# Kernel tuning notes

Measured on AMD Instinct MI355X. Metric: run time of the kernel, lower is better.

The kernel has to match this reference:

```python
import jax, jax.numpy as jnp
import numpy as np

N = 4096
D_IN = 1024
D_OUT = 1024
NUM_HEADS = 16
HEAD_DIM = D_OUT // NUM_HEADS


def setup_inputs() -> dict:
    key = jax.random.key(0)
    ks = jax.random.split(key, 7)
    scale = 1.0 / np.sqrt(D_IN)
    return {
        "q": jax.random.normal(ks[0], (N, D_IN), dtype=jnp.float32),
        "k": jax.random.normal(ks[1], (N, D_IN), dtype=jnp.float32),
        "v": jax.random.normal(ks[2], (N, D_IN), dtype=jnp.float32),
        "W_q": jax.random.normal(ks[3], (D_IN, D_OUT), dtype=jnp.float32) * scale,
        "W_k": jax.random.normal(ks[4], (D_IN, D_OUT), dtype=jnp.float32) * scale,
        "W_v": jax.random.normal(ks[5], (D_IN, D_OUT), dtype=jnp.float32) * scale,
        "W_o": jax.random.normal(ks[6], (D_OUT, D_OUT), dtype=jnp.float32) * scale,
    }


def reference(q, k, v, W_q, W_k, W_v, W_o):
    n = q.shape[0]
    # QKV projections -> [h, n, d]
    Q = (q @ W_q).reshape(n, NUM_HEADS, HEAD_DIM).transpose(1, 0, 2)
    K = (k @ W_k).reshape(n, NUM_HEADS, HEAD_DIM).transpose(1, 0, 2)
    V = (v @ W_v).reshape(n, NUM_HEADS, HEAD_DIM).transpose(1, 0, 2)
    scores = jnp.einsum('hid,hjd->hij', Q, K) / jnp.sqrt(jnp.float32(HEAD_DIM))
    attn = jax.nn.softmax(scores, axis=-1)  # dropout p=0.0 (eval) -> no-op
    h = jnp.einsum('hij,hjd->hid', attn, V)
    h = h.transpose(1, 0, 2).reshape(n, D_OUT)
    return h @ W_o
```

## Files before the change

### kernel.cpp

```cpp
#include <hip/hip_runtime.h>
#include <math.h>

#define NTOK   4096
#define DMODEL 1024
#define NHEADS 16
#define HDIM   64
#define KDIM   1024

typedef __attribute__((ext_vector_type(8))) short          bf16x8;
typedef __attribute__((ext_vector_type(4))) float          f32x4;
typedef __attribute__((ext_vector_type(4))) unsigned short us4;

static __device__ __forceinline__ unsigned short f2bf(float f) {
    unsigned int u = __float_as_uint(f);
    u += 0x7fffu + ((u >> 16) & 1u);
    return (unsigned short)(u >> 16);
}

static __device__ __forceinline__ unsigned int pkbf(float a, float b) {
    unsigned int ua = __float_as_uint(a) + 0x8000u;
    unsigned int ub = __float_as_uint(b) + 0x8000u;
    return __builtin_amdgcn_perm(ub, ua, 0x07060302u);
}

#if __has_builtin(__builtin_amdgcn_exp2f)
#define EXP2(x) __builtin_amdgcn_exp2f(x)
#else
#define EXP2(x) exp2f(x)
#endif

static __device__ __forceinline__ void async_copy16(void* lds, const void* g) {
    __builtin_amdgcn_global_load_lds(
        (const __attribute__((address_space(1))) unsigned int*)g,
        (__attribute__((address_space(3))) unsigned int*)lds, 16, 0, 0);
}

__global__ __launch_bounds__(256)
void cast_wt_kernel(const float* __restrict__ Wq, const float* __restrict__ Wk,
                    const float* __restrict__ Wv, const float* __restrict__ Wo,
                    unsigned short* __restrict__ Tq, unsigned short* __restrict__ Tk,
                    unsigned short* __restrict__ Tv, unsigned short* __restrict__ To) {
    __shared__ float Ws[64][65];
    const float* W;
    unsigned short* T;
    switch (blockIdx.z) {
        case 0:  W = Wq; T = Tq; break;
        case 1:  W = Wk; T = Tk; break;
        case 2:  W = Wv; T = Tv; break;
        default: W = Wo; T = To; break;
    }
    const int k0 = blockIdx.x * 64, n0 = blockIdx.y * 64;
    const int t = threadIdx.x;
    #pragma unroll
    for (int i = 0; i < 4; i++) {
        int c  = i * 256 + t;
        int kk = c >> 4;
        int n4 = (c & 15) << 2;
        *(float4*)(&Ws[kk][n4]) =
            *(const float4*)(W + (size_t)(k0 + kk) * DMODEL + n0 + n4);
    }
    __syncthreads();
    #pragma unroll
    for (int i = 0; i < 4; i++) {
        int c  = i * 256 + t;
        int nn = c >> 4;
        int k4 = (c & 15) << 2;
        us4 o = { f2bf(Ws[k4 + 0][nn]), f2bf(Ws[k4 + 1][nn]),
                  f2bf(Ws[k4 + 2][nn]), f2bf(Ws[k4 + 3][nn]) };
        *(us4*)(T + (size_t)(n0 + nn) * KDIM + k0 + k4) = o;
    }
}

__global__ __launch_bounds__(256, 3)
void qkv_gemm(const float* __restrict__ Aq, const float* __restrict__ Ak,
              const float* __restrict__ Av,
              const unsigned short* __restrict__ Btq,
              const unsigned short* __restrict__ Btk,
              const unsigned short* __restrict__ Btv,
              unsigned short* __restrict__ Oq, unsigned short* __restrict__ Ok,
              unsigned short* __restrict__ Ov) {
    __shared__ unsigned short As[128 * 64];
    __shared__ unsigned short Bs[128 * 64];

    const float* A;
    const unsigned short* Bt;
    unsigned short* Out;
    int mode;
    float sc;
    switch (blockIdx.z) {
        case 0:  A = Aq; Bt = Btq; Out = Oq; mode = 1; sc = 0.18033688011112042f; break;
        case 1:  A = Ak; Bt = Btk; Out = Ok; mode = 1; sc = 1.0f;   break;
        default: A = Av; Bt = Btv; Out = Ov; mode = 2; sc = 1.0f;   break;
    }

    const int t    = threadIdx.x;
    const int w    = t >> 6;
    const int lane = t & 63;
    const int quad = lane >> 4;
    const int l15  = lane & 15;
    const int wr   = w >> 1, wc = w & 1;
    const int bm   = blockIdx.y * 128, bn = blockIdx.x * 128;

    f32x4 acc[4][4];
    #pragma unroll
    for (int i = 0; i < 4; i++)
        #pragma unroll
        for (int j = 0; j < 4; j++) acc[i][j] = (f32x4)(0.f);

    for (int k0 = 0; k0 < KDIM; k0 += 64) {
        __syncthreads();
        #pragma unroll
        for (int i = 0; i < 4; i++) {
            int cb = (i * 4 + w) * 64;
            int c  = cb + lane;
            int r  = c >> 3;
            int ko = (c & 7) * 8;
            async_copy16((void*)(Bs + cb * 8),
                         (const void*)(Bt + (size_t)(bn + r) * KDIM + k0 + ko));
        }
        #pragma unroll
        for (int i = 0; i < 4; i++) {
            int c2 = i * 256 + t;
            int r  = c2 >> 3;
            int k8 = (c2 & 7) * 8;
            const float* src = A + (size_t)(bm + r) * KDIM + k0 + k8;
            float4 f0 = *(const float4*)(src);
            float4 f1 = *(const float4*)(src + 4);
            bf16x8 pk = { (short)f2bf(f0.x), (short)f2bf(f0.y),
                          (short)f2bf(f0.z), (short)f2bf(f0.w),
                          (short)f2bf(f1.x), (short)f2bf(f1.y),
                          (short)f2bf(f1.z), (short)f2bf(f1.w) };
            *(bf16x8*)(As + r * 64 + k8) = pk;
        }
        __syncthreads();
        #pragma unroll
        for (int kq = 0; kq < 2; kq++) {
            bf16x8 af[4], bf[4];
            #pragma unroll
            for (int mt = 0; mt < 4; mt++)
                af[mt] = *(bf16x8*)(As + (wr * 64 + mt * 16 + l15) * 64 + kq * 32 + quad * 8);
            #pragma unroll
            for (int nt = 0; nt < 4; nt++)
                bf[nt] = *(bf16x8*)(Bs + (wc * 64 + nt * 16 + l15) * 64 + kq * 32 + quad * 8);
            #pragma unroll
            for (int mt = 0; mt < 4; mt++)
                #pragma unroll
                for (int nt = 0; nt < 4; nt++)
                    acc[mt][nt] = __builtin_amdgcn_mfma_f32_16x16x32_bf16(
                        af[mt], bf[nt], acc[mt][nt], 0, 0, 0);
        }
    }

    #pragma unroll
    for (int mt = 0; mt < 4; mt++) {
        #pragma unroll
        for (int nt = 0; nt < 4; nt++) {
            int col  = bn + wc * 64 + nt * 16 + l15;
            int row0 = bm + wr * 64 + mt * 16 + quad * 4;
            if (mode == 1) {
                size_t base = ((size_t)(col >> 6)) * NTOK * HDIM + (col & 63);
                #pragma unroll
                for (int r = 0; r < 4; r++)
                    Out[base + (size_t)(row0 + r) * HDIM] = f2bf(acc[mt][nt][r] * sc);
            } else {
                size_t base = ((size_t)(col >> 6)) * HDIM * NTOK +
                              (size_t)(col & 63) * NTOK + row0;
                us4 o = { f2bf(acc[mt][nt][0]), f2bf(acc[mt][nt][1]),
                          f2bf(acc[mt][nt][2]), f2bf(acc[mt][nt][3]) };
                *(us4*)(Out + base) = o;
            }
        }
    }
}

__global__ __launch_bounds__(256, 3)
void out_gemm(const unsigned short* __restrict__ A,
              const unsigned short* __restrict__ Bt,
              float* __restrict__ Out) {
    __shared__ unsigned short As[128 * 64];
    __shared__ unsigned short Bs[128 * 64];

    const int t    = threadIdx.x;
    const int w    = t >> 6;
    const int lane = t & 63;
    const int quad = lane >> 4;
    const int l15  = lane & 15;
    const int wr   = w >> 1, wc = w & 1;
    const int bm   = blockIdx.y * 128, bn = blockIdx.x * 128;

    f32x4 acc[4][4];
    #pragma unroll
    for (int i = 0; i < 4; i++)
        #pragma unroll
        for (int j = 0; j < 4; j++) acc[i][j] = (f32x4)(0.f);

    for (int k0 = 0; k0 < KDIM; k0 += 64) {
        __syncthreads();
        #pragma unroll
        for (int i = 0; i < 4; i++) {
            int cb = (i * 4 + w) * 64;
            int c  = cb + lane;
            int r  = c >> 3;
            int ko = (c & 7) * 8;
            async_copy16((void*)(Bs + cb * 8),
                         (const void*)(Bt + (size_t)(bn + r) * KDIM + k0 + ko));
            async_copy16((void*)(As + cb * 8),
                         (const void*)(A + (size_t)(bm + r) * KDIM + k0 + ko));
        }
        __syncthreads();
        #pragma unroll
        for (int kq = 0; kq < 2; kq++) {
            bf16x8 af[4], bf[4];
            #pragma unroll
            for (int mt = 0; mt < 4; mt++)
                af[mt] = *(bf16x8*)(As + (wr * 64 + mt * 16 + l15) * 64 + kq * 32 + quad * 8);
            #pragma unroll
            for (int nt = 0; nt < 4; nt++)
                bf[nt] = *(bf16x8*)(Bs + (wc * 64 + nt * 16 + l15) * 64 + kq * 32 + quad * 8);
            #pragma unroll
            for (int mt = 0; mt < 4; mt++)
                #pragma unroll
                for (int nt = 0; nt < 4; nt++)
                    acc[mt][nt] = __builtin_amdgcn_mfma_f32_16x16x32_bf16(
                        af[mt], bf[nt], acc[mt][nt], 0, 0, 0);
        }
    }

    #pragma unroll
    for (int mt = 0; mt < 4; mt++) {
        #pragma unroll
        for (int nt = 0; nt < 4; nt++) {
            int col  = bn + wc * 64 + nt * 16 + l15;
            int row0 = bm + wr * 64 + mt * 16 + quad * 4;
            #pragma unroll
            for (int r = 0; r < 4; r++)
                Out[(size_t)(row0 + r) * DMODEL + col] = acc[mt][nt][r];
        }
    }
}

__global__ __launch_bounds__(256)
void attn_mfma(const unsigned short* __restrict__ Q,
               const unsigned short* __restrict__ K,
               const unsigned short* __restrict__ Vt,
               unsigned short* __restrict__ ctx) {
    __shared__ __align__(16) unsigned short Ks[2 * 4096];
    __shared__ __align__(16) unsigned short Vs[2 * 4096];
    __shared__ __align__(16) unsigned short Ps[4][32][72];

    const int h    = blockIdx.y;
    const int qt   = blockIdx.x;
    const int t    = threadIdx.x;
    const int w    = t >> 6;
    const int lane = t & 63;
    const int quad = lane >> 4;
    const int l15  = lane & 15;

    const unsigned short* Qg =
        Q + ((size_t)h * NTOK + qt * 128 + w * 32 + l15) * HDIM;
    bf16x8 qf[2][2];
    qf[0][0] = *(const bf16x8*)(Qg + quad * 8);
    qf[0][1] = *(const bf16x8*)(Qg + 32 + quad * 8);
    qf[1][0] = *(const bf16x8*)(Qg + 16 * HDIM + quad * 8);
    qf[1][1] = *(const bf16x8*)(Qg + 16 * HDIM + 32 + quad * 8);

    const unsigned short* Kg = K  + (size_t)h * NTOK * HDIM;
    const unsigned short* Vg = Vt + (size_t)h * HDIM * NTOK;

    const int xb = l15 & 7;
    const int a0 = l15 * 64 + ((quad    ) ^ xb) * 8;
    const int a1 = l15 * 64 + ((quad + 4) ^ xb) * 8;

    auto stage = [&](int kt, int b) {
        #pragma unroll
        for (int i = 0; i < 2; i++) {
            int c = i * 256 + t;
            int r = c >> 3;
            int o = ((c & 7) ^ (r & 7)) * 8;
            async_copy16((void*)(Ks + b * 4096 + (i * 256 + w * 64) * 8),
                         (const void*)(Kg + (size_t)(kt * 64 + r) * HDIM + o));
            async_copy16((void*)(Vs + b * 4096 + (i * 256 + w * 64) * 8),
                         (const void*)(Vg + (size_t)r * NTOK + kt * 64 + o));
        }
    };

    f32x4 O[2][4];
    float l_part[2] = {0.f, 0.f};
    #pragma unroll
    for (int tl = 0; tl < 2; tl++)
        #pragma unroll
        for (int dt = 0; dt < 4; dt++) O[tl][dt] = (f32x4)(0.f);

    stage(0, 0);

    for (int kt = 0; kt < NTOK / 64; kt++) {
        const int cur = kt & 1;
        __syncthreads();
        if (kt + 1 < NTOK / 64) stage(kt + 1, cur ^ 1);

        f32x4 s[2][4];
        #pragma unroll
        for (int kc = 0; kc < 4; kc++) {
            bf16x8 kf0 = *(bf16x8*)(Ks + cur * 4096 + kc * 1024 + a0);
            bf16x8 kf1 = *(bf16x8*)(Ks + cur * 4096 + kc * 1024 + a1);
            #pragma unroll
            for (int tl = 0; tl < 2; tl++) {
                f32x4 acc = (f32x4)(0.f);
                acc = __builtin_amdgcn_mfma_f32_16x16x32_bf16(kf0, qf[tl][0], acc, 0, 0, 0);
                acc = __builtin_amdgcn_mfma_f32_16x16x32_bf16(kf1, qf[tl][1], acc, 0, 0, 0);
                s[tl][kc] = acc;
            }
        }

        #pragma unroll
        for (int tl = 0; tl < 2; tl++) {
            float sm = 0.f;
            #pragma unroll
            for (int kc = 0; kc < 4; kc++) {
                float e0 = EXP2(s[tl][kc][0]);
                float e1 = EXP2(s[tl][kc][1]);
                float e2 = EXP2(s[tl][kc][2]);
                float e3 = EXP2(s[tl][kc][3]);
                sm += (e0 + e1) + (e2 + e3);
                uint2 p = { pkbf(e0, e1), pkbf(e2, e3) };
                *(uint2*)(&Ps[w][tl * 16 + l15][kc * 16 + quad * 4]) = p;
            }
            l_part[tl] += sm;
        }
        asm volatile("s_waitcnt lgkmcnt(0)" ::: "memory");

        bf16x8 pf[2][2];
        #pragma unroll
        for (int tl = 0; tl < 2; tl++) {
            pf[tl][0] = *(bf16x8*)(&Ps[w][tl * 16 + l15][quad * 8]);
            pf[tl][1] = *(bf16x8*)(&Ps[w][tl * 16 + l15][32 + quad * 8]);
        }
        #pragma unroll
        for (int dt = 0; dt < 4; dt++) {
            bf16x8 vf0 = *(bf16x8*)(Vs + cur * 4096 + dt * 1024 + a0);
            bf16x8 vf1 = *(bf16x8*)(Vs + cur * 4096 + dt * 1024 + a1);
            #pragma unroll
            for (int tl = 0; tl < 2; tl++) {
                O[tl][dt] = __builtin_amdgcn_mfma_f32_16x16x32_bf16(vf0, pf[tl][0], O[tl][dt], 0, 0, 0);
                O[tl][dt] = __builtin_amdgcn_mfma_f32_16x16x32_bf16(vf1, pf[tl][1], O[tl][dt], 0, 0, 0);
            }
        }
    }

    #pragma unroll
    for (int tl = 0; tl < 2; tl++) {
        float ls = l_part[tl];
        ls += __shfl_xor(ls, 16, 64);
        ls += __shfl_xor(ls, 32, 64);
        float inv = 1.f / ls;
        size_t row = (size_t)qt * 128 + w * 32 + tl * 16 + l15;
        #pragma unroll
        for (int dt = 0; dt < 4; dt++) {
            uint2 o = { pkbf(O[tl][dt][0] * inv, O[tl][dt][1] * inv),
                        pkbf(O[tl][dt][2] * inv, O[tl][dt][3] * inv) };
            *(uint2*)(ctx + row * DMODEL + h * HDIM + dt * 16 + quad * 4) = o;
        }
    }
}

extern "C" void kernel_launch(void* const* d_in, const int* in_sizes, int n_in,
                              void* d_out, int out_size, void* d_ws, size_t ws_size,
                              hipStream_t stream) {
    const float* q  = (const float*)d_in[0];
    const float* k  = (const float*)d_in[1];
    const float* v  = (const float*)d_in[2];
    const float* Wq = (const float*)d_in[3];
    const float* Wk = (const float*)d_in[4];
    const float* Wv = (const float*)d_in[5];
    const float* Wo = (const float*)d_in[6];
    float* out = (float*)d_out;

    unsigned short* WqT = (unsigned short*)d_ws;
    unsigned short* WkT = WqT + (size_t)DMODEL * KDIM;
    unsigned short* WvT = WkT + (size_t)DMODEL * KDIM;
    unsigned short* WoT = WvT + (size_t)DMODEL * KDIM;
    unsigned short* Qh  = WoT + (size_t)DMODEL * KDIM;
    unsigned short* Kh  = Qh  + (size_t)NTOK * DMODEL;
    unsigned short* Vth = Kh  + (size_t)NTOK * DMODEL;
    unsigned short* ctx = Vth + (size_t)NTOK * DMODEL;

    cast_wt_kernel<<<dim3(16, 16, 4), 256, 0, stream>>>(Wq, Wk, Wv, Wo,
                                                        WqT, WkT, WvT, WoT);
    qkv_gemm<<<dim3(DMODEL / 128, NTOK / 128, 3), 256, 0, stream>>>(
        q, k, v, WqT, WkT, WvT, Qh, Kh, Vth);
    attn_mfma<<<dim3(NTOK / 128, NHEADS), 256, 0, stream>>>(Qh, Kh, Vth, ctx);
    out_gemm<<<dim3(DMODEL / 128, NTOK / 128), 256, 0, stream>>>(ctx, WoT, out);
}
```

Before: 296.1 us.

## Precast activations to bf16, use hardware bf16 pack, MFMA row sums in attention

Adds a separate cast kernel that converts q/k/v to bf16 so the QKV GEMM can load its A tiles with async global-to-LDS copies instead of converting in registers. This path is only taken when the workspace is large enough. Packed bf16 conversion now uses the hardware cvt_pk builtin where the compiler provides it. In attention, the softmax row sums are computed with an MFMA against a ones vector instead of scalar adds and shuffles, the K/V staging addresses are simplified, and V fragments are preloaded with per-tile waits. The cost is an extra kernel launch plus a round trip of the activations through bf16 memory.

```diff
diff --git a/kernel.cpp b/kernel.cpp
--- a/kernel.cpp
+++ b/kernel.cpp
@@ -17,10 +17,15 @@
     return (unsigned short)(u >> 16);
 }
 
-static __device__ __forceinline__ unsigned int pkbf(float a, float b) {
+static __device__ __forceinline__ unsigned int pk2bf(float a, float b) {
+#if __has_builtin(__builtin_amdgcn_cvt_pk_bf16_f32)
+    return __builtin_bit_cast(unsigned int,
+                              __builtin_amdgcn_cvt_pk_bf16_f32(a, b));
+#else
     unsigned int ua = __float_as_uint(a) + 0x8000u;
     unsigned int ub = __float_as_uint(b) + 0x8000u;
     return __builtin_amdgcn_perm(ub, ua, 0x07060302u);
+#endif
 }
 
 #if __has_builtin(__builtin_amdgcn_exp2f)
@@ -71,26 +76,49 @@
     }
 }
 
+__global__ __launch_bounds__(256)
+void cast_in_kernel(const float* __restrict__ q, const float* __restrict__ k,
+                    const float* __restrict__ v,
+                    unsigned short* __restrict__ Qb,
+                    unsigned short* __restrict__ Kb,
+                    unsigned short* __restrict__ Vb) {
+    const float* src;
+    unsigned short* dst;
+    switch (blockIdx.y) {
+        case 0:  src = q; dst = Qb; break;
+        case 1:  src = k; dst = Kb; break;
+        default: src = v; dst = Vb; break;
+    }
+    size_t i = ((size_t)blockIdx.x * 256 + threadIdx.x) * 8;
+    float4 f0 = *(const float4*)(src + i);
+    float4 f1 = *(const float4*)(src + i + 4);
+    uint2 o0 = { pk2bf(f0.x, f0.y), pk2bf(f0.z, f0.w) };
+    uint2 o1 = { pk2bf(f1.x, f1.y), pk2bf(f1.z, f1.w) };
+    *(uint2*)(dst + i)     = o0;
+    *(uint2*)(dst + i + 4) = o1;
+}
+
 __global__ __launch_bounds__(256, 3)
-void qkv_gemm(const float* __restrict__ Aq, const float* __restrict__ Ak,
-              const float* __restrict__ Av,
-              const unsigned short* __restrict__ Btq,
-              const unsigned short* __restrict__ Btk,
-              const unsigned short* __restrict__ Btv,
-              unsigned short* __restrict__ Oq, unsigned short* __restrict__ Ok,
-              unsigned short* __restrict__ Ov) {
+void qkv_gemm_pre(const unsigned short* __restrict__ Qb,
+                  const unsigned short* __restrict__ Kb,
+                  const unsigned short* __restrict__ Vb,
+                  const unsigned short* __restrict__ Btq,
+                  const unsigned short* __restrict__ Btk,
+                  const unsigned short* __restrict__ Btv,
+                  unsigned short* __restrict__ Oq, unsigned short* __restrict__ Ok,
+                  unsigned short* __restrict__ Ov) {
     __shared__ unsigned short As[128 * 64];
     __shared__ unsigned short Bs[128 * 64];
 
-    const float* A;
+    const unsigned short* A;
     const unsigned short* Bt;
     unsigned short* Out;
     int mode;
     float sc;
     switch (blockIdx.z) {
-        case 0:  A = Aq; Bt = Btq; Out = Oq; mode = 1; sc = 0.18033688011112042f; break;
-        case 1:  A = Ak; Bt = Btk; Out = Ok; mode = 1; sc = 1.0f;   break;
-        default: A = Av; Bt = Btv; Out = Ov; mode = 2; sc = 1.0f;   break;
+        case 0:  A = Qb; Bt = Btq; Out = Oq; mode = 1; sc = 0.18033688011112042f; break;
+        case 1:  A = Kb; Bt = Btk; Out = Ok; mode = 1; sc = 1.0f; break;
+        default: A = Vb; Bt = Btv; Out = Ov; mode = 2; sc = 1.0f; break;
     }
 
     const int t    = threadIdx.x;
@@ -117,20 +145,8 @@
             int ko = (c & 7) * 8;
             async_copy16((void*)(Bs + cb * 8),
                          (const void*)(Bt + (size_t)(bn + r) * KDIM + k0 + ko));
-        }
-        #pragma unroll
-        for (int i = 0; i < 4; i++) {
-            int c2 = i * 256 + t;
-            int r  = c2 >> 3;
-            int k8 = (c2 & 7) * 8;
-            const float* src = A + (size_t)(bm + r) * KDIM + k0 + k8;
-            float4 f0 = *(const float4*)(src);
-            float4 f1 = *(const float4*)(src + 4);
-            bf16x8 pk = { (short)f2bf(f0.x), (short)f2bf(f0.y),
-                          (short)f2bf(f0.z), (short)f2bf(f0.w),
-                          (short)f2bf(f1.x), (short)f2bf(f1.y),
-                          (short)f2bf(f1.z), (short)f2bf(f1.w) };
-            *(bf16x8*)(As + r * 64 + k8) = pk;
+            async_copy16((void*)(As + cb * 8),
+                         (const void*)(A + (size_t)(bm + r) * KDIM + k0 + ko));
         }
         __syncthreads();
         #pragma unroll
@@ -174,6 +190,107 @@
 }
 
 __global__ __launch_bounds__(256, 3)
+void qkv_gemm(const float* __restrict__ Aq, const float* __restrict__ Ak,
+              const float* __restrict__ Av,
+              const unsigned short* __restrict__ Btq,
+              const unsigned short* __restrict__ Btk,
+              const unsigned short* __restrict__ Btv,
+              unsigned short* __restrict__ Oq, unsigned short* __restrict__ Ok,
+              unsigned short* __restrict__ Ov) {
+    __shared__ unsigned short As[128 * 64];
+    __shared__ unsigned short Bs[128 * 64];
+
+    const float* A;
+    const unsigned short* Bt;
+    unsigned short* Out;
+    int mode;
+    float sc;
+    switch (blockIdx.z) {
+        case 0:  A = Aq; Bt = Btq; Out = Oq; mode = 1; sc = 0.18033688011112042f; break;
+        case 1:  A = Ak; Bt = Btk; Out = Ok; mode = 1; sc = 1.0f; break;
+        default: A = Av; Bt = Btv; Out = Ov; mode = 2; sc = 1.0f; break;
+    }
+
+    const int t    = threadIdx.x;
+    const int w    = t >> 6;
+    const int lane = t & 63;
+    const int quad = lane >> 4;
+    const int l15  = lane & 15;
+    const int wr   = w >> 1, wc = w & 1;
+    const int bm   = blockIdx.y * 128, bn = blockIdx.x * 128;
+
+    f32x4 acc[4][4];
+    #pragma unroll
+    for (int i = 0; i < 4; i++)
+        #pragma unroll
+        for (int j = 0; j < 4; j++) acc[i][j] = (f32x4)(0.f);
+
+    for (int k0 = 0; k0 < KDIM; k0 += 64) {
+        __syncthreads();
+        #pragma unroll
+        for (int i = 0; i < 4; i++) {
+            int cb = (i * 4 + w) * 64;
+            int c  = cb + lane;
+            int r  = c >> 3;
+            int ko = (c & 7) * 8;
+            async_copy16((void*)(Bs + cb * 8),
+                         (const void*)(Bt + (size_t)(bn + r) * KDIM + k0 + ko));
+        }
+        #pragma unroll
+        for (int i = 0; i < 4; i++) {
+            int c2 = i * 256 + t;
+            int r  = c2 >> 3;
+            int k8 = (c2 & 7) * 8;
+            const float* src = A + (size_t)(bm + r) * KDIM + k0 + k8;
+            float4 f0 = *(const float4*)(src);
+            float4 f1 = *(const float4*)(src + 4);
+            uint2 p0 = { pk2bf(f0.x, f0.y), pk2bf(f0.z, f0.w) };
+            uint2 p1 = { pk2bf(f1.x, f1.y), pk2bf(f1.z, f1.w) };
+            *(uint2*)(As + r * 64 + k8)     = p0;
+            *(uint2*)(As + r * 64 + k8 + 4) = p1;
+        }
+        __syncthreads();
+        #pragma unroll
+        for (int kq = 0; kq < 2; kq++) {
+            bf16x8 af[4], bf[4];
+            #pragma unroll
+            for (int mt = 0; mt < 4; mt++)
+                af[mt] = *(bf16x8*)(As + (wr * 64 + mt * 16 + l15) * 64 + kq * 32 + quad * 8);
+            #pragma unroll
+            for (int nt = 0; nt < 4; nt++)
+                bf[nt] = *(bf16x8*)(Bs + (wc * 64 + nt * 16 + l15) * 64 + kq * 32 + quad * 8);
+            #pragma unroll
+            for (int mt = 0; mt < 4; mt++)
+                #pragma unroll
+                for (int nt = 0; nt < 4; nt++)
+                    acc[mt][nt] = __builtin_amdgcn_mfma_f32_16x16x32_bf16(
+                        af[mt], bf[nt], acc[mt][nt], 0, 0, 0);
+        }
+    }
+
+    #pragma unroll
+    for (int mt = 0; mt < 4; mt++) {
+        #pragma unroll
+        for (int nt = 0; nt < 4; nt++) {
+            int col  = bn + wc * 64 + nt * 16 + l15;
+            int row0 = bm + wr * 64 + mt * 16 + quad * 4;
+            if (mode == 1) {
+                size_t base = ((size_t)(col >> 6)) * NTOK * HDIM + (col & 63);
+                #pragma unroll
+                for (int r = 0; r < 4; r++)
+                    Out[base + (size_t)(row0 + r) * HDIM] = f2bf(acc[mt][nt][r] * sc);
+            } else {
+                size_t base = ((size_t)(col >> 6)) * HDIM * NTOK +
+                              (size_t)(col & 63) * NTOK + row0;
+                us4 o = { f2bf(acc[mt][nt][0]), f2bf(acc[mt][nt][1]),
+                          f2bf(acc[mt][nt][2]), f2bf(acc[mt][nt][3]) };
+                *(us4*)(Out + base) = o;
+            }
+        }
+    }
+}
+
+__global__ __launch_bounds__(256, 3)
 void out_gemm(const unsigned short* __restrict__ A,
               const unsigned short* __restrict__ Bt,
               float* __restrict__ Out) {
@@ -267,29 +384,37 @@
     const unsigned short* Kg = K  + (size_t)h * NTOK * HDIM;
     const unsigned short* Vg = Vt + (size_t)h * HDIM * NTOK;
 
+    const int rr = t >> 3;
+    const int oo = ((t & 7) ^ (rr & 7)) * 8;
+    const unsigned short* kbase = Kg + (size_t)rr * HDIM + oo;
+    const unsigned short* vbase = Vg + (size_t)rr * NTOK + oo;
+    unsigned short* ksd = Ks + w * 512;
+    unsigned short* vsd = Vs + w * 512;
+
+    auto stage = [&](int kt, int b) {
+        const unsigned short* kp = kbase + (size_t)kt * 64 * HDIM;
+        const unsigned short* vp = vbase + kt * 64;
+        async_copy16((void*)(ksd + b * 4096),        (const void*)kp);
+        async_copy16((void*)(ksd + b * 4096 + 2048), (const void*)(kp + 32 * HDIM));
+        async_copy16((void*)(vsd + b * 4096),        (const void*)vp);
+        async_copy16((void*)(vsd + b * 4096 + 2048), (const void*)(vp + (size_t)32 * NTOK));
+    };
+
     const int xb = l15 & 7;
     const int a0 = l15 * 64 + ((quad    ) ^ xb) * 8;
     const int a1 = l15 * 64 + ((quad + 4) ^ xb) * 8;
 
-    auto stage = [&](int kt, int b) {
-        #pragma unroll
-        for (int i = 0; i < 2; i++) {
-            int c = i * 256 + t;
-            int r = c >> 3;
-            int o = ((c & 7) ^ (r & 7)) * 8;
-            async_copy16((void*)(Ks + b * 4096 + (i * 256 + w * 64) * 8),
-                         (const void*)(Kg + (size_t)(kt * 64 + r) * HDIM + o));
-            async_copy16((void*)(Vs + b * 4096 + (i * 256 + w * 64) * 8),
-                         (const void*)(Vg + (size_t)r * NTOK + kt * 64 + o));
-        }
-    };
+    const bf16x8 ones = { 16256, 16256, 16256, 16256,
+                          16256, 16256, 16256, 16256 };
 
     f32x4 O[2][4];
-    float l_part[2] = {0.f, 0.f};
-    #pragma unroll
-    for (int tl = 0; tl < 2; tl++)
+    f32x4 lacc[2];
+    #pragma unroll
+    for (int tl = 0; tl < 2; tl++) {
+        lacc[tl] = (f32x4)(0.f);
         #pragma unroll
         for (int dt = 0; dt < 4; dt++) O[tl][dt] = (f32x4)(0.f);
+    }
 
     stage(0, 0);
 
@@ -312,52 +437,46 @@
             }
         }
 
+        bf16x8 vf[4][2];
+        #pragma unroll
+        for (int dt = 0; dt < 4; dt++) {
+            vf[dt][0] = *(bf16x8*)(Vs + cur * 4096 + dt * 1024 + a0);
+            vf[dt][1] = *(bf16x8*)(Vs + cur * 4096 + dt * 1024 + a1);
+        }
+
         #pragma unroll
         for (int tl = 0; tl < 2; tl++) {
-            float sm = 0.f;
             #pragma unroll
             for (int kc = 0; kc < 4; kc++) {
                 float e0 = EXP2(s[tl][kc][0]);
                 float e1 = EXP2(s[tl][kc][1]);
                 float e2 = EXP2(s[tl][kc][2]);
                 float e3 = EXP2(s[tl][kc][3]);
-                sm += (e0 + e1) + (e2 + e3);
-                uint2 p = { pkbf(e0, e1), pkbf(e2, e3) };
+                uint2 p = { pk2bf(e0, e1), pk2bf(e2, e3) };
                 *(uint2*)(&Ps[w][tl * 16 + l15][kc * 16 + quad * 4]) = p;
             }
-            l_part[tl] += sm;
-        }
-        asm volatile("s_waitcnt lgkmcnt(0)" ::: "memory");
-
-        bf16x8 pf[2][2];
-        #pragma unroll
-        for (int tl = 0; tl < 2; tl++) {
-            pf[tl][0] = *(bf16x8*)(&Ps[w][tl * 16 + l15][quad * 8]);
-            pf[tl][1] = *(bf16x8*)(&Ps[w][tl * 16 + l15][32 + quad * 8]);
-        }
+            asm volatile("s_waitcnt lgkmcnt(0)" ::: "memory");
+
+            bf16x8 pf0 = *(bf16x8*)(&Ps[w][tl * 16 + l15][quad * 8]);
+            bf16x8 pf1 = *(bf16x8*)(&Ps[w][tl * 16 + l15][32 + quad * 8]);
+            lacc[tl] = __builtin_amdgcn_mfma_f32_16x16x32_bf16(ones, pf0, lacc[tl], 0, 0, 0);
+            lacc[tl] = __builtin_amdgcn_mfma_f32_16x16x32_bf16(ones, pf1, lacc[tl], 0, 0, 0);
+            #pragma unroll
+            for (int dt = 0; dt < 4; dt++) {
+                O[tl][dt] = __builtin_amdgcn_mfma_f32_16x16x32_bf16(vf[dt][0], pf0, O[tl][dt], 0, 0, 0);
+                O[tl][dt] = __builtin_amdgcn_mfma_f32_16x16x32_bf16(vf[dt][1], pf1, O[tl][dt], 0, 0, 0);
+            }
+        }
+    }
+
+    #pragma unroll
+    for (int tl = 0; tl < 2; tl++) {
+        float inv = 1.f / lacc[tl][0];
+        size_t row = (size_t)qt * 128 + w * 32 + tl * 16 + l15;
         #pragma unroll
         for (int dt = 0; dt < 4; dt++) {
-            bf16x8 vf0 = *(bf16x8*)(Vs + cur * 4096 + dt * 1024 + a0);
-            bf16x8 vf1 = *(bf16x8*)(Vs + cur * 4096 + dt * 1024 + a1);
-            #pragma unroll
-            for (int tl = 0; tl < 2; tl++) {
-                O[tl][dt] = __builtin_amdgcn_mfma_f32_16x16x32_bf16(vf0, pf[tl][0], O[tl][dt], 0, 0, 0);
-                O[tl][dt] = __builtin_amdgcn_mfma_f32_16x16x32_bf16(vf1, pf[tl][1], O[tl][dt], 0, 0, 0);
-            }
-        }
-    }
-
-    #pragma unroll
-    for (int tl = 0; tl < 2; tl++) {
-        float ls = l_part[tl];
-        ls += __shfl_xor(ls, 16, 64);
-        ls += __shfl_xor(ls, 32, 64);
-        float inv = 1.f / ls;
-        size_t row = (size_t)qt * 128 + w * 32 + tl * 16 + l15;
-        #pragma unroll
-        for (int dt = 0; dt < 4; dt++) {
-            uint2 o = { pkbf(O[tl][dt][0] * inv, O[tl][dt][1] * inv),
-                        pkbf(O[tl][dt][2] * inv, O[tl][dt][3] * inv) };
+            uint2 o = { pk2bf(O[tl][dt][0] * inv, O[tl][dt][1] * inv),
+                        pk2bf(O[tl][dt][2] * inv, O[tl][dt][3] * inv) };
             *(uint2*)(ctx + row * DMODEL + h * HDIM + dt * 16 + quad * 4) = o;
         }
     }
@@ -383,11 +502,22 @@
     unsigned short* Kh  = Qh  + (size_t)NTOK * DMODEL;
     unsigned short* Vth = Kh  + (size_t)NTOK * DMODEL;
     unsigned short* ctx = Vth + (size_t)NTOK * DMODEL;
+    unsigned short* Qb  = ctx + (size_t)NTOK * DMODEL;
+    unsigned short* Kb  = Qb  + (size_t)NTOK * DMODEL;
+    unsigned short* Vb  = Kb  + (size_t)NTOK * DMODEL;
+
+    const bool precast = ws_size >= (size_t)67108864;
 
     cast_wt_kernel<<<dim3(16, 16, 4), 256, 0, stream>>>(Wq, Wk, Wv, Wo,
                                                         WqT, WkT, WvT, WoT);
-    qkv_gemm<<<dim3(DMODEL / 128, NTOK / 128, 3), 256, 0, stream>>>(
-        q, k, v, WqT, WkT, WvT, Qh, Kh, Vth);
+    if (precast) {
+        cast_in_kernel<<<dim3(2048, 3), 256, 0, stream>>>(q, k, v, Qb, Kb, Vb);
+        qkv_gemm_pre<<<dim3(DMODEL / 128, NTOK / 128, 3), 256, 0, stream>>>(
+            Qb, Kb, Vb, WqT, WkT, WvT, Qh, Kh, Vth);
+    } else {
+        qkv_gemm<<<dim3(DMODEL / 128, NTOK / 128, 3), 256, 0, stream>>>(
+            q, k, v, WqT, WkT, WvT, Qh, Kh, Vth);
+    }
     attn_mfma<<<dim3(NTOK / 128, NHEADS), 256, 0, stream>>>(Qh, Kh, Vth, ctx);
     out_gemm<<<dim3(DMODEL / 128, NTOK / 128), 256, 0, stream>>>(ctx, WoT, out);
 }
```

Result: faster. 277.4 us (-6.3%).
